# Kernel tuning notes

Measured on AMD Instinct MI355X. Metric: run time of the kernel, lower is better.

The kernel has to match this reference:

```python
import jax, jax.numpy as jnp
import numpy as np

MAX_GRAD = 200.0


@jax.custom_vjp
def sqrt_bound_derivative(x):
    return jnp.sqrt(x)


def _sqrt_bd_fwd(x):
    return jnp.sqrt(x), x


def _sqrt_bd_bwd(x, g):
    # derivative of sqrt clipped to MAX_GRAD: 0.5/sqrt(x) <= MAX_GRAD  <=>  x >= 1/(4*MAX_GRAD^2)
    x_clipped = jnp.maximum(x, 1.0 / (4.0 * MAX_GRAD * MAX_GRAD))
    return (g * 0.5 / jnp.sqrt(x_clipped),)


sqrt_bound_derivative.defvjp(_sqrt_bd_fwd, _sqrt_bd_bwd)


def linear_scan(a, x, h0):
    # h_t = a_t * h_{t-1} + x_t, diagonal recurrence over axis=1 (time).
    # Parallel form via associative scan on pairs (a, b): combine -> (a1*a2, a2*b1 + b2).
    def combine(c1, c2):
        a1, b1 = c1
        a2, b2 = c2
        return a1 * a2, a2 * b1 + b2

    a_cum, h = jax.lax.associative_scan(combine, (a, x), axis=1)
    # fold in initial state: h_t += (prod_{u<=t} a_u) * h0
    h = h + a_cum * h0[:, None, :]
    return h, h[:, -1]


def setup_inputs() -> dict:
    key = jax.random.key(0)
    ks = jax.random.split(key, 8)
    B, S, D_IN, D_HID, D_OUT = 8, 4096, 512, 1024, 512
    R_MIN, R_MAX = 0.9, 0.999

    x = jax.random.normal(ks[0], (B, S, D_IN), dtype=jnp.float32)
    h0 = jnp.zeros((B, D_HID), dtype=jnp.float32)

    # stable_init: a_logit = logit(U(r_min, r_max)) so that a = sigmoid(a_logit) in [r_min, r_max]
    u = jax.random.uniform(ks[1], (D_HID,), minval=R_MIN, maxval=R_MAX)
    a_logit = jnp.log(u) - jnp.log1p(-u)

    def dense_init(k, d_in, d_out):
        scale = 1.0 / np.sqrt(d_in)
        return jax.random.uniform(k, (d_in, d_out), minval=-scale, maxval=scale).astype(jnp.float32)

    W_dx = dense_init(ks[2], D_IN, D_OUT)
    b_dx = jnp.zeros((D_OUT,), dtype=jnp.float32)
    W_in = dense_init(ks[3], D_IN, D_HID)
    b_in = jnp.zeros((D_HID,), dtype=jnp.float32)
    W_out = dense_init(ks[4], D_HID, D_OUT)
    b_out = jnp.zeros((D_OUT,), dtype=jnp.float32)

    return {"x": x, "h0": h0, "a_logit": a_logit,
            "W_dx": W_dx, "b_dx": b_dx,
            "W_in": W_in, "b_in": b_in,
            "W_out": W_out, "b_out": b_out}


def reference(x, h0, a_logit, W_dx, b_dx, W_in, b_in, W_out, b_out):
    a = jax.nn.sigmoid(a_logit)                      # (d_hidden,)
    dx = jnp.einsum('bsi,io->bso', x, W_dx) + b_dx   # skip projection (b, s, d_out)
    u = jnp.einsum('bsi,ih->bsh', x, W_in) + b_in    # input projection (b, s, d_hidden)
    u = sqrt_bound_derivative(1.0 - a * a) * u       # input_norm gating
    a_b = jnp.broadcast_to(a, u.shape)
    h, h_last = linear_scan(a_b, u, h0)              # diagonal linear recurrence
    out = (dx + jnp.einsum('bsh,ho->bso', h, W_out) + b_out) / 2.0
    return out, h_last
```

## Files before the change

kernel.cpp:

```cpp
#include <hip/hip_runtime.h>

#define B_    8
#define S_    4096
#define DIN   512
#define DHID  1024
#define DOUT  512
#define M_    (B_*S_)
#define NCAT  (DHID + DOUT)
#define CH2   32
#define NCH2  (S_/CH2)

typedef __bf16 bf16x8 __attribute__((ext_vector_type(8)));
typedef float  floatx4 __attribute__((ext_vector_type(4)));

__device__ __forceinline__ unsigned short f2bf(float f) {
  unsigned u = __builtin_bit_cast(unsigned, f);
  u = (u + 0x7FFFu + ((u >> 16) & 1u)) >> 16;
  return (unsigned short)u;
}
__device__ __forceinline__ float bf2f(unsigned short h) {
  unsigned u = ((unsigned)h) << 16;
  return __builtin_bit_cast(float, u);
}

__device__ __forceinline__ void gl_lds16(const unsigned short* g, unsigned short* l) {
  __builtin_amdgcn_global_load_lds((const __attribute__((address_space(1))) void*)g,
                                   (__attribute__((address_space(3))) void*)l, 16, 0, 0);
}

__global__ void prep_all(const float* __restrict__ logit,
                         const float* __restrict__ Win, const float* __restrict__ Wdx,
                         const float* __restrict__ Wout, const float* __restrict__ x,
                         float* __restrict__ a_s,
                         unsigned short* __restrict__ wcat,
                         unsigned short* __restrict__ woutt,
                         unsigned short* __restrict__ xb) {
  int bx = blockIdx.x;
  if (bx < 3072) {
    int idx = bx * 256 + threadIdx.x;
    int n = idx >> 9, k = idx & 511;
    float v = (n < DHID) ? Win[(size_t)k * DHID + n] : Wdx[(size_t)k * DOUT + (n - DHID)];
    wcat[idx] = f2bf(v);
  } else if (bx < 5120) {
    int idx = (bx - 3072) * 256 + threadIdx.x;
    int n = idx >> 10, k = idx & 1023;
    woutt[idx] = f2bf(Wout[(size_t)k * DOUT + n]);
  } else if (bx < 5124) {
    int d = (bx - 5120) * 256 + threadIdx.x;
    if (d < DHID) {
      float a = 1.f / (1.f + expf(-logit[d]));
      a_s[d] = a;
      a_s[DHID + d] = sqrtf(fmaxf(1.f - a * a, 0.f));
    }
  } else {
    size_t i = (size_t)(bx - 5124) * 256 + threadIdx.x;
    const float4* p = (const float4*)x;
    float4 v0 = p[i * 2];
    float4 v1 = p[i * 2 + 1];
    uint4 o;
    o.x = (unsigned)f2bf(v0.x) | ((unsigned)f2bf(v0.y) << 16);
    o.y = (unsigned)f2bf(v0.z) | ((unsigned)f2bf(v0.w) << 16);
    o.z = (unsigned)f2bf(v1.x) | ((unsigned)f2bf(v1.y) << 16);
    o.w = (unsigned)f2bf(v1.z) | ((unsigned)f2bf(v1.w) << 16);
    *(uint4*)&xb[i * 8] = o;
  }
}

template <int K, int MODE, int NB>
__global__ __launch_bounds__(256, 4) void gemm_bt(
    const unsigned short* __restrict__ A,
    const unsigned short* __restrict__ Bt,
    const float* __restrict__ a_s,
    const float* __restrict__ bias0,
    const float* __restrict__ bias1,
    unsigned short* __restrict__ u_out,
    unsigned short* __restrict__ dx_buf,
    float* __restrict__ out,
    float* __restrict__ carry)
{
  __shared__ __align__(16) unsigned char smem[32768];
  unsigned short* lA = (unsigned short*)smem;
  unsigned short* lB = (unsigned short*)(smem + 16384);
  float* stg  = (float*)smem;
  float* ltmp = (float*)(smem + 16896);

  const int tid = threadIdx.x;
  const int flat = blockIdx.y * gridDim.x + blockIdx.x;
  const int xcd = flat & 7;
  const int j = flat >> 3;
  const int n0 = (j % NB) * 128;
  const int m0 = ((j / NB) * 8 + xcd) * 128;

  const int wid = tid >> 6, lane = tid & 63;
  const int wm = (wid >> 1) * 64, wn = (wid & 1) * 64;
  const int r16 = lane & 15, quad = lane >> 4;
  const int sw = r16 & 7;

  const int rsub = lane >> 3;
  const int gcol = ((lane & 7) ^ rsub) << 3;

  const unsigned short* Abase = A + (size_t)(m0 + (wid << 5) + rsub) * K + gcol;
  const unsigned short* Bbase = Bt + (size_t)(n0 + (wid << 5) + rsub) * K + gcol;
  unsigned short* lAw = lA + (wid << 5) * 64;
  unsigned short* lBw = lB + (wid << 5) * 64;

  floatx4 acc[4][4] = {};

  for (int k0 = 0; k0 < K; k0 += 64) {
#pragma unroll
    for (int i = 0; i < 4; ++i) {
      gl_lds16(Abase + (size_t)(i * 8) * K + k0, lAw + i * 8 * 64);
      gl_lds16(Bbase + (size_t)(i * 8) * K + k0, lBw + i * 8 * 64);
    }
    __syncthreads();
#pragma unroll
    for (int ks = 0; ks < 2; ++ks) {
      bf16x8 af[4], bfr[4];
#pragma unroll
      for (int i = 0; i < 4; ++i)
        af[i] = *(const bf16x8*)&lA[(wm + i * 16 + r16) * 64 + ((((ks << 2) | quad) ^ sw) << 3)];
#pragma unroll
      for (int j2 = 0; j2 < 4; ++j2)
        bfr[j2] = *(const bf16x8*)&lB[(wn + j2 * 16 + r16) * 64 + ((((ks << 2) | quad) ^ sw) << 3)];
#pragma unroll
      for (int i = 0; i < 4; ++i)
#pragma unroll
        for (int j2 = 0; j2 < 4; ++j2)
          acc[i][j2] = __builtin_amdgcn_mfma_f32_16x16x32_bf16(af[i], bfr[j2], acc[i][j2], 0, 0, 0);
    }
    __syncthreads();
  }

  const int row = tid >> 3;
  const int seg = tid & 7;
  const int scol_ = tid & 127;
  const int shalf = tid >> 7;
  float aa = 0.f, sbi = 0.f, ssc = 0.f, a16 = 0.f;
  if (MODE == 0 && n0 < DHID) {
    aa  = a_s[n0 + scol_];
    sbi = bias0[n0 + scol_];
    ssc = a_s[DHID + n0 + scol_];
    float t2 = aa * aa, t4 = t2 * t2, t8 = t4 * t4;
    a16 = t8 * t8;
  }
  const int bb = m0 >> 12;
  const int c0 = (m0 & 4095) >> 5;

#pragma unroll
  for (int p = 0; p < 4; ++p) {
    __syncthreads();
    if ((wid >> 1) == (p >> 1)) {
      const int i0 = (p & 1) * 2;
#pragma unroll
      for (int ii = 0; ii < 2; ++ii) {
        const int i = i0 + ii;
        const int srow = i * 16 + quad * 4 - (p & 1) * 32;
#pragma unroll
        for (int j2 = 0; j2 < 4; ++j2) {
          const int scol = wn + j2 * 16 + r16;
#pragma unroll
          for (int r = 0; r < 4; ++r)
            stg[(srow + r) * 132 + scol] = acc[i][j2][r];
        }
      }
    }
    __syncthreads();

    if (MODE == 0 && n0 < DHID) {
      float P = 0.f;
      const float* sp = &stg[(shalf * 16) * 132 + scol_];
#pragma unroll
      for (int r = 0; r < 16; ++r) {
        P = fmaf(aa, P, (sp[0] + sbi) * ssc);
        sp += 132;
      }
      if (shalf) ltmp[scol_] = P;
      __syncthreads();
      if (!shalf)
        carry[((size_t)bb * NCH2 + c0 + p) * DHID + n0 + scol_] = fmaf(a16, P, ltmp[scol_]);
    }

    const int gm = m0 + p * 32 + row;
    const int col0 = n0 + seg * 16;
    if (MODE == 0) {
      union { unsigned short s[16]; uint4 q[2]; } ub;
      if (n0 < DHID) {
#pragma unroll
        for (int u = 0; u < 4; ++u) {
          float4 v  = *(const float4*)&stg[row * 132 + seg * 16 + u * 4];
          float4 bi = *(const float4*)&bias0[col0 + u * 4];
          float4 sc = *(const float4*)&a_s[DHID + col0 + u * 4];
          ub.s[u * 4 + 0] = f2bf((v.x + bi.x) * sc.x);
          ub.s[u * 4 + 1] = f2bf((v.y + bi.y) * sc.y);
          ub.s[u * 4 + 2] = f2bf((v.z + bi.z) * sc.z);
          ub.s[u * 4 + 3] = f2bf((v.w + bi.w) * sc.w);
        }
        *(uint4*)&u_out[(size_t)gm * DHID + col0]     = ub.q[0];
        *(uint4*)&u_out[(size_t)gm * DHID + col0 + 8] = ub.q[1];
      } else {
        const int c2 = col0 - DHID;
#pragma unroll
        for (int u = 0; u < 4; ++u) {
          float4 v  = *(const float4*)&stg[row * 132 + seg * 16 + u * 4];
          float4 bd = *(const float4*)&bias1[c2 + u * 4];
          ub.s[u * 4 + 0] = f2bf(v.x + bd.x);
          ub.s[u * 4 + 1] = f2bf(v.y + bd.y);
          ub.s[u * 4 + 2] = f2bf(v.z + bd.z);
          ub.s[u * 4 + 3] = f2bf(v.w + bd.w);
        }
        *(uint4*)&dx_buf[(size_t)gm * DOUT + c2]     = ub.q[0];
        *(uint4*)&dx_buf[(size_t)gm * DOUT + c2 + 8] = ub.q[1];
      }
    } else {
#pragma unroll
      for (int u = 0; u < 4; ++u) {
        float4 v  = *(const float4*)&stg[row * 132 + seg * 16 + u * 4];
        float4 bo = *(const float4*)&bias0[col0 + u * 4];
        ushort4 dv = *(const ushort4*)&dx_buf[(size_t)gm * DOUT + col0 + u * 4];
        float4 o;
        o.x = (v.x + bo.x + bf2f(dv.x)) * 0.5f;
        o.y = (v.y + bo.y + bf2f(dv.y)) * 0.5f;
        o.z = (v.z + bo.z + bf2f(dv.z)) * 0.5f;
        o.w = (v.w + bo.w + bf2f(dv.w)) * 0.5f;
        *(float4*)&out[(size_t)gm * DOUT + col0 + u * 4] = o;
      }
    }
  }
}

__global__ __launch_bounds__(256) void scan_mid(const float* __restrict__ a_s,
                                                const float* __restrict__ h0,
                                                float* __restrict__ carry,
                                                float* __restrict__ h_last) {
  int idx = blockIdx.x * 256 + threadIdx.x;
  int d = idx & (DHID - 1);
  int b = idx >> 10;
  float a = a_s[d];
  float aL = a;
#pragma unroll
  for (int q = 0; q < 5; ++q) aL *= aL;
  float st = h0[(size_t)b * DHID + d];
  float* p = &carry[(size_t)b * NCH2 * DHID + d];
  for (int cg = 0; cg < NCH2; cg += 8) {
    float loc[8];
#pragma unroll
    for (int j = 0; j < 8; ++j) loc[j] = p[(size_t)j * DHID];
#pragma unroll
    for (int j = 0; j < 8; ++j) {
      p[(size_t)j * DHID] = st;
      st = fmaf(aL, st, loc[j]);
    }
    p += (size_t)8 * DHID;
  }
  h_last[(size_t)b * DHID + d] = st;
}

__global__ __launch_bounds__(256) void scan2(unsigned short* __restrict__ u,
                                             const float* __restrict__ a_s,
                                             const float* __restrict__ carry) {
  int idx = blockIdx.x * 256 + threadIdx.x;
  int d8 = (idx & 127) * 8;
  int c  = (idx >> 7) & (NCH2 - 1);
  int b  = idx >> 14;
  float4 a0 = *(const float4*)&a_s[d8];
  float4 a1 = *(const float4*)&a_s[d8 + 4];
  const float* cp = &carry[((size_t)(b * NCH2 + c)) * DHID + d8];
  float4 e0 = *(const float4*)cp;
  float4 e1 = *(const float4*)(cp + 4);
  float h0_ = e0.x, h1 = e0.y, h2 = e0.z, h3 = e0.w;
  float h4 = e1.x, h5 = e1.y, h6 = e1.z, h7 = e1.w;
  unsigned short* up = u + ((size_t)(b * S_ + c * CH2)) * DHID + d8;
#pragma unroll 4
  for (int t = 0; t < CH2; ++t) {
    ushort4 q0 = *(const ushort4*)up;
    ushort4 q1 = *(const ushort4*)(up + 4);
    h0_ = fmaf(a0.x, h0_, bf2f(q0.x)); h1 = fmaf(a0.y, h1, bf2f(q0.y));
    h2  = fmaf(a0.z, h2,  bf2f(q0.z)); h3 = fmaf(a0.w, h3, bf2f(q0.w));
    h4  = fmaf(a1.x, h4,  bf2f(q1.x)); h5 = fmaf(a1.y, h5, bf2f(q1.y));
    h6  = fmaf(a1.z, h6,  bf2f(q1.z)); h7 = fmaf(a1.w, h7, bf2f(q1.w));
    ushort4 w0, w1;
    w0.x = f2bf(h0_); w0.y = f2bf(h1); w0.z = f2bf(h2); w0.w = f2bf(h3);
    w1.x = f2bf(h4);  w1.y = f2bf(h5); w1.z = f2bf(h6); w1.w = f2bf(h7);
    *(ushort4*)up = w0;
    *(ushort4*)(up + 4) = w1;
    up += DHID;
  }
}

extern "C" void kernel_launch(void* const* d_in, const int* in_sizes, int n_in,
                              void* d_out, int out_size, void* d_ws, size_t ws_size,
                              hipStream_t stream) {
  const float* x    = (const float*)d_in[0];
  const float* h0   = (const float*)d_in[1];
  const float* alog = (const float*)d_in[2];
  const float* Wdx  = (const float*)d_in[3];
  const float* bdx  = (const float*)d_in[4];
  const float* Win  = (const float*)d_in[5];
  const float* bin  = (const float*)d_in[6];
  const float* Wout = (const float*)d_in[7];
  const float* bout = (const float*)d_in[8];

  float* out    = (float*)d_out;
  float* h_last = out + (size_t)M_ * DOUT;

  char* ws = (char*)d_ws;
  unsigned short* xb    = (unsigned short*)(ws);
  unsigned short* ubuf  = (unsigned short*)(ws + 33554432ull);
  unsigned short* dxb   = (unsigned short*)(ws + 100663296ull);
  unsigned short* wcat  = (unsigned short*)(ws + 134217728ull);
  unsigned short* woutt = (unsigned short*)(ws + 135790592ull);
  float*          a_s   = (float*)(ws + 136839168ull);
  float*          carry = (float*)(ws + 136847360ull);

  prep_all<<<5124 + (M_ * DIN / 8) / 256, 256, 0, stream>>>(
      alog, Win, Wdx, Wout, x, a_s, wcat, woutt, xb);

  gemm_bt<DIN, 0, 12><<<dim3(NCAT / 128, M_ / 128), 256, 0, stream>>>(
      xb, wcat, a_s, bin, bdx, ubuf, dxb, nullptr, carry);

  scan_mid<<<(B_ * DHID) / 256, 256, 0, stream>>>(a_s, h0, carry, h_last);
  scan2   <<<(B_ * NCH2 * (DHID / 8)) / 256, 256, 0, stream>>>(ubuf, a_s, carry);

  gemm_bt<DHID, 1, 4><<<dim3(DOUT / 128, M_ / 128), 256, 0, stream>>>(
      ubuf, woutt, a_s, bout, nullptr, nullptr, dxb, out, nullptr);
}
```

Baseline: 283.3 us.

## Replace first GEMM with 256x256-tile, 512-thread, 4-stage pipelined kernel

Adds a dedicated first-projection kernel that uses 256x256 output tiles with 8 waves, a 4-slot direct global-to-LDS staging pipeline and swizzled LDS reads. Its block index is remapped so that neighbouring blocks share tiles for better cache locality. The epilogue stages results through LDS in four passes to compute the chunk carries and write bf16 u/dx. The goal is more data reuse per loaded byte and better overlap of memory with MFMA work, at the cost of 128KB LDS per block and heavy register use, which lower occupancy.

Result: no change. 278.5 us (-1.7%).

```diff
diff --git a/kernel.cpp b/kernel.cpp
--- a/kernel.cpp
+++ b/kernel.cpp
@@ -63,6 +63,178 @@
     o.z = (unsigned)f2bf(v1.x) | ((unsigned)f2bf(v1.y) << 16);
     o.w = (unsigned)f2bf(v1.z) | ((unsigned)f2bf(v1.w) << 16);
     *(uint4*)&xb[i * 8] = o;
+  }
+}
+
+__global__ __launch_bounds__(512, 2) void gemm1(
+    const unsigned short* __restrict__ A,
+    const unsigned short* __restrict__ Bt,
+    const float* __restrict__ a_s,
+    const float* __restrict__ bin,
+    const float* __restrict__ bdx,
+    unsigned short* __restrict__ u_out,
+    unsigned short* __restrict__ dx_buf,
+    float* __restrict__ carry)
+{
+  __shared__ __align__(16) unsigned char smem[131072];
+
+  const int tid  = threadIdx.x;
+  const int lane = tid & 63, wid = tid >> 6;
+  const int r16  = lane & 15, quad = lane >> 4;
+  const int wm = (wid >> 2) * 128, wn = (wid & 3) * 64;
+  const int csw = (quad ^ ((r16 >> 1) & 3)) << 4;
+
+  const int flat = blockIdx.x;
+  const int jj = (flat & 7) * 96 + (flat >> 3);
+  const int nt = jj % 6, mt = jj / 6;
+  const int n0 = nt * 256, m0 = mt * 256;
+
+  const unsigned oA0 = (unsigned)wid * 1024u + (unsigned)lane * 16u;
+  const unsigned oA1 = oA0 + 8192u;
+  const int rA0 = oA0 >> 6, cA0 = (int)((oA0 >> 4) & 3u) ^ ((rA0 >> 1) & 3);
+  const int rA1 = oA1 >> 6, cA1 = (int)((oA1 >> 4) & 3u) ^ ((rA1 >> 1) & 3);
+  const unsigned short* sA0 = A  + (size_t)(m0 + rA0) * DIN + cA0 * 8;
+  const unsigned short* sA1 = A  + (size_t)(m0 + rA1) * DIN + cA1 * 8;
+  const unsigned short* sB0 = Bt + (size_t)(n0 + rA0) * DIN + cA0 * 8;
+  const unsigned short* sB1 = Bt + (size_t)(n0 + rA1) * DIN + cA1 * 8;
+
+  unsigned char* lds = smem;
+  const unsigned dA0 = (unsigned)wid * 1024u, dA1 = dA0 + 8192u;
+
+  floatx4 acc[8][4] = {};
+
+  auto stage = [&](int slot, int kt) {
+    unsigned char* d = lds + slot * 32768;
+    const int ko = kt * 32;
+    gl_lds16(sA0 + ko, (unsigned short*)(d + dA0));
+    gl_lds16(sA1 + ko, (unsigned short*)(d + dA1));
+    gl_lds16(sB0 + ko, (unsigned short*)(d + 16384 + dA0));
+    gl_lds16(sB1 + ko, (unsigned short*)(d + 16384 + dA1));
+  };
+
+  auto compute = [&](int slot) {
+    const unsigned char* pA = lds + slot * 32768;
+    const unsigned char* pB = pA + 16384;
+    bf16x8 af[8], bfr[4];
+#pragma unroll
+    for (int j = 0; j < 4; ++j)
+      bfr[j] = *(const bf16x8*)(pB + (wn + j * 16 + r16) * 64 + csw);
+#pragma unroll
+    for (int i = 0; i < 8; ++i)
+      af[i] = *(const bf16x8*)(pA + (wm + i * 16 + r16) * 64 + csw);
+    __builtin_amdgcn_s_setprio(1);
+#pragma unroll
+    for (int i = 0; i < 8; ++i)
+#pragma unroll
+      for (int j = 0; j < 4; ++j)
+        acc[i][j] = __builtin_amdgcn_mfma_f32_16x16x32_bf16(af[i], bfr[j], acc[i][j], 0, 0, 0);
+    __builtin_amdgcn_s_setprio(0);
+  };
+
+  stage(0, 0); stage(1, 1); stage(2, 2);
+  asm volatile("s_waitcnt vmcnt(8)" ::: "memory");
+  __builtin_amdgcn_s_barrier();
+
+  for (int t = 0; t < 13; ++t) {
+    stage((t + 3) & 3, t + 3);
+    compute(t & 3);
+    asm volatile("s_waitcnt vmcnt(8) lgkmcnt(0)" ::: "memory");
+    __builtin_amdgcn_s_barrier();
+  }
+  compute(1);
+  asm volatile("s_waitcnt vmcnt(4) lgkmcnt(0)" ::: "memory");
+  __builtin_amdgcn_s_barrier();
+  compute(2);
+  asm volatile("s_waitcnt vmcnt(0) lgkmcnt(0)" ::: "memory");
+  __builtin_amdgcn_s_barrier();
+  compute(3);
+  asm volatile("s_waitcnt lgkmcnt(0)" ::: "memory");
+  __builtin_amdgcn_s_barrier();
+
+  float* stg = (float*)smem;
+  const bool isU = (n0 < DHID);
+
+  const int sg = tid & 31, rw0 = tid >> 5;
+  const int colS = tid & 255, ch = tid >> 8;
+
+  float aa = 0.f, sbi = 0.f, ssc = 0.f;
+  float4 bv0, bv1, sv0, sv1;
+  if (isU) {
+    aa  = a_s[n0 + colS];
+    sbi = bin[n0 + colS];
+    ssc = a_s[DHID + n0 + colS];
+    bv0 = *(const float4*)&bin[n0 + sg * 8];
+    bv1 = *(const float4*)&bin[n0 + sg * 8 + 4];
+    sv0 = *(const float4*)&a_s[DHID + n0 + sg * 8];
+    sv1 = *(const float4*)&a_s[DHID + n0 + sg * 8 + 4];
+  } else {
+    bv0 = *(const float4*)&bdx[n0 - DHID + sg * 8];
+    bv1 = *(const float4*)&bdx[n0 - DHID + sg * 8 + 4];
+    sv0 = bv0; sv1 = bv1;
+  }
+
+#pragma unroll
+  for (int p = 0; p < 4; ++p) {
+    if ((wid >> 2) == (p >> 1)) {
+      const int ib = (p & 1) * 4;
+#pragma unroll
+      for (int ii = 0; ii < 4; ++ii) {
+#pragma unroll
+        for (int j = 0; j < 4; ++j) {
+          const int col = (wid & 3) * 64 + j * 16 + r16;
+#pragma unroll
+          for (int r = 0; r < 4; ++r)
+            stg[(ii * 16 + quad * 4 + r) * 260 + col] = acc[ib + ii][j][r];
+        }
+      }
+    }
+    asm volatile("s_waitcnt lgkmcnt(0)" ::: "memory");
+    __builtin_amdgcn_s_barrier();
+
+    const int gmb = m0 + p * 64;
+    if (isU) {
+      float P = 0.f;
+      const float* sp = &stg[(ch * 32) * 260 + colS];
+#pragma unroll
+      for (int r = 0; r < 32; ++r) { P = fmaf(aa, P, (sp[0] + sbi) * ssc); sp += 260; }
+      const int gm0 = gmb + ch * 32;
+      carry[((size_t)(gm0 >> 12) * NCH2 + ((gm0 & 4095) >> 5)) * DHID + n0 + colS] = P;
+#pragma unroll
+      for (int q = 0; q < 4; ++q) {
+        const int lr = rw0 + q * 16;
+        float4 v0 = *(const float4*)&stg[lr * 260 + sg * 8];
+        float4 v1 = *(const float4*)&stg[lr * 260 + sg * 8 + 4];
+        union { unsigned short s[8]; uint4 u4; } ub;
+        ub.s[0] = f2bf((v0.x + bv0.x) * sv0.x);
+        ub.s[1] = f2bf((v0.y + bv0.y) * sv0.y);
+        ub.s[2] = f2bf((v0.z + bv0.z) * sv0.z);
+        ub.s[3] = f2bf((v0.w + bv0.w) * sv0.w);
+        ub.s[4] = f2bf((v1.x + bv1.x) * sv1.x);
+        ub.s[5] = f2bf((v1.y + bv1.y) * sv1.y);
+        ub.s[6] = f2bf((v1.z + bv1.z) * sv1.z);
+        ub.s[7] = f2bf((v1.w + bv1.w) * sv1.w);
+        *(uint4*)&u_out[(size_t)(gmb + lr) * DHID + n0 + sg * 8] = ub.u4;
+      }
+    } else {
+#pragma unroll
+      for (int q = 0; q < 4; ++q) {
+        const int lr = rw0 + q * 16;
+        float4 v0 = *(const float4*)&stg[lr * 260 + sg * 8];
+        float4 v1 = *(const float4*)&stg[lr * 260 + sg * 8 + 4];
+        union { unsigned short s[8]; uint4 u4; } ub;
+        ub.s[0] = f2bf(v0.x + bv0.x);
+        ub.s[1] = f2bf(v0.y + bv0.y);
+        ub.s[2] = f2bf(v0.z + bv0.z);
+        ub.s[3] = f2bf(v0.w + bv0.w);
+        ub.s[4] = f2bf(v1.x + bv1.x);
+        ub.s[5] = f2bf(v1.y + bv1.y);
+        ub.s[6] = f2bf(v1.z + bv1.z);
+        ub.s[7] = f2bf(v1.w + bv1.w);
+        *(uint4*)&dx_buf[(size_t)(gmb + lr) * DOUT + (n0 - DHID) + sg * 8] = ub.u4;
+      }
+    }
+    asm volatile("s_waitcnt lgkmcnt(0)" ::: "memory");
+    __builtin_amdgcn_s_barrier();
   }
 }
 
@@ -315,8 +487,8 @@
   prep_all<<<5124 + (M_ * DIN / 8) / 256, 256, 0, stream>>>(
       alog, Win, Wdx, Wout, x, a_s, wcat, woutt, xb);
 
-  gemm_bt<DIN, 0, 12><<<dim3(NCAT / 128, M_ / 128), 256, 0, stream>>>(
-      xb, wcat, a_s, bin, bdx, ubuf, dxb, nullptr, carry);
+  gemm1<<<dim3((M_ / 256) * (NCAT / 256)), dim3(512), 0, stream>>>(
+      xb, wcat, a_s, bin, bdx, ubuf, dxb, carry);
 
   scan_mid<<<(B_ * DHID) / 256, 256, 0, stream>>>(a_s, h0, carry, h_last);
   scan2   <<<(B_ * NCH2 * (DHID / 8)) / 256, 256, 0, stream>>>(ubuf, a_s, carry);
```

## Replace 128x128 GEMM with 256x256 tile, 4-stage LDS pipelined kernel

Applied to the files above, without the earlier changes.

Both GEMMs move from a 128x128 tile with 256 threads to a 256x256 tile with 512 threads (8 waves). K-slices of 32 are loaded into a 4-deep LDS ring, staged three slices ahead, with hand-placed barriers, vmcnt waits and setprio around the MFMA bursts. The epilogue is rewritten for the larger tile, and the per-chunk carry is now computed by one thread over 32 rows. The aim is more data reuse per tile and better overlap of global loads with MFMA, at the cost of 128KB LDS per block, lower occupancy, and fragile manual synchronisation.

Measured after the change: 270.2 us. -4.6%, faster.

```diff
diff --git a/kernel.cpp b/kernel.cpp
--- a/kernel.cpp
+++ b/kernel.cpp
@@ -66,8 +66,8 @@
   }
 }
 
-template <int K, int MODE, int NB>
-__global__ __launch_bounds__(256, 4) void gemm_bt(
+template <int K, int MODE, int NTN>
+__global__ __launch_bounds__(512, 2) void gemm256(
     const unsigned short* __restrict__ A,
     const unsigned short* __restrict__ Bt,
     const float* __restrict__ a_s,
@@ -75,156 +75,185 @@
     const float* __restrict__ bias1,
     unsigned short* __restrict__ u_out,
     unsigned short* __restrict__ dx_buf,
+    const unsigned short* __restrict__ dx_in,
     float* __restrict__ out,
     float* __restrict__ carry)
 {
-  __shared__ __align__(16) unsigned char smem[32768];
-  unsigned short* lA = (unsigned short*)smem;
-  unsigned short* lB = (unsigned short*)(smem + 16384);
-  float* stg  = (float*)smem;
-  float* ltmp = (float*)(smem + 16896);
-
-  const int tid = threadIdx.x;
-  const int flat = blockIdx.y * gridDim.x + blockIdx.x;
-  const int xcd = flat & 7;
-  const int j = flat >> 3;
-  const int n0 = (j % NB) * 128;
-  const int m0 = ((j / NB) * 8 + xcd) * 128;
-
-  const int wid = tid >> 6, lane = tid & 63;
-  const int wm = (wid >> 1) * 64, wn = (wid & 1) * 64;
-  const int r16 = lane & 15, quad = lane >> 4;
-  const int sw = r16 & 7;
-
-  const int rsub = lane >> 3;
-  const int gcol = ((lane & 7) ^ rsub) << 3;
-
-  const unsigned short* Abase = A + (size_t)(m0 + (wid << 5) + rsub) * K + gcol;
-  const unsigned short* Bbase = Bt + (size_t)(n0 + (wid << 5) + rsub) * K + gcol;
-  unsigned short* lAw = lA + (wid << 5) * 64;
-  unsigned short* lBw = lB + (wid << 5) * 64;
-
-  floatx4 acc[4][4] = {};
-
-  for (int k0 = 0; k0 < K; k0 += 64) {
-#pragma unroll
-    for (int i = 0; i < 4; ++i) {
-      gl_lds16(Abase + (size_t)(i * 8) * K + k0, lAw + i * 8 * 64);
-      gl_lds16(Bbase + (size_t)(i * 8) * K + k0, lBw + i * 8 * 64);
+  constexpr int NG = K / 32;
+  __shared__ __align__(16) unsigned char smem[131072];
+  unsigned char* lds = smem;
+
+  const int tid  = threadIdx.x;
+  const int lane = tid & 63, wid = tid >> 6;
+  const int r16  = lane & 15, quad = lane >> 4;
+  const int wm = (wid >> 2) * 128, wn = (wid & 3) * 64;
+  const int csw = (quad ^ ((r16 >> 1) & 3)) << 4;
+
+  constexpr int TOT = (M_ / 256) * NTN;
+  const int flat = blockIdx.x;
+  const int jj = (flat & 7) * (TOT / 8) + (flat >> 3);
+  const int nt = jj % NTN, mt = jj / NTN;
+  const int n0 = nt * 256, m0 = mt * 256;
+
+  const int srow = (wid << 4) + (lane >> 2);
+  const int scol = ((lane & 3) ^ ((lane >> 3) & 3)) << 3;
+  const unsigned short* gA0 = A  + (size_t)(m0 + srow) * K + scol;
+  const unsigned short* gB0 = Bt + (size_t)(n0 + srow) * K + scol;
+  const unsigned oA = (unsigned)wid * 1024u + (unsigned)lane * 16u;
+
+  floatx4 acc[8][4] = {};
+  bf16x8 af[4], bf[4];
+
+  auto stageA = [&](int g) {
+    unsigned short* d = (unsigned short*)(lds + (g & 3) * 32768 + oA);
+    const unsigned short* s = gA0 + (size_t)g * 32;
+    gl_lds16(s, d);
+    gl_lds16(s + (size_t)128 * K, d + 4096);
+  };
+  auto stageB = [&](int g) {
+    unsigned short* d = (unsigned short*)(lds + (g & 3) * 32768 + 16384 + oA);
+    const unsigned short* s = gB0 + (size_t)g * 32;
+    gl_lds16(s, d);
+    gl_lds16(s + (size_t)128 * K, d + 4096);
+  };
+
+  auto phA = [&](int g, int gs, bool st) {
+    const unsigned char* sl = lds + (g & 3) * 32768;
+#pragma unroll
+    for (int j = 0; j < 4; ++j)
+      bf[j] = *(const bf16x8*)(sl + 16384 + (wn + j * 16 + r16) * 64 + csw);
+#pragma unroll
+    for (int i = 0; i < 4; ++i)
+      af[i] = *(const bf16x8*)(sl + (wm + i * 16 + r16) * 64 + csw);
+    if (st) stageA(gs);
+    asm volatile("s_barrier" ::: "memory");
+    asm volatile("s_waitcnt lgkmcnt(0)" ::: "memory");
+    __builtin_amdgcn_sched_barrier(0);
+    __builtin_amdgcn_s_setprio(1);
+#pragma unroll
+    for (int i = 0; i < 4; ++i)
+#pragma unroll
+      for (int j = 0; j < 4; ++j)
+        acc[i][j] = __builtin_amdgcn_mfma_f32_16x16x32_bf16(af[i], bf[j], acc[i][j], 0, 0, 0);
+    __builtin_amdgcn_s_setprio(0);
+    asm volatile("s_barrier" ::: "memory");
+  };
+  auto phB = [&](int g, int gs, bool st) {
+    const unsigned char* sl = lds + (g & 3) * 32768;
+#pragma unroll
+    for (int i = 0; i < 4; ++i)
+      af[i] = *(const bf16x8*)(sl + (wm + (4 + i) * 16 + r16) * 64 + csw);
+    if (st) stageB(gs);
+    asm volatile("s_barrier" ::: "memory");
+    asm volatile("s_waitcnt lgkmcnt(0)" ::: "memory");
+    __builtin_amdgcn_sched_barrier(0);
+    __builtin_amdgcn_s_setprio(1);
+#pragma unroll
+    for (int i = 0; i < 4; ++i)
+#pragma unroll
+      for (int j = 0; j < 4; ++j)
+        acc[4 + i][j] = __builtin_amdgcn_mfma_f32_16x16x32_bf16(af[i], bf[j], acc[4 + i][j], 0, 0, 0);
+    __builtin_amdgcn_s_setprio(0);
+  };
+
+  stageA(0); stageB(0); stageA(1); stageB(1); stageA(2); stageB(2);
+  asm volatile("s_waitcnt vmcnt(8)" ::: "memory");
+  asm volatile("s_barrier" ::: "memory");
+
+  for (int g = 0; g < NG - 3; ++g) {
+    phA(g, g + 3, true);
+    phB(g, g + 3, true);
+    asm volatile("s_waitcnt vmcnt(8)" ::: "memory");
+    asm volatile("s_barrier" ::: "memory");
+  }
+  phA(NG - 3, 0, false); phB(NG - 3, 0, false);
+  asm volatile("s_waitcnt vmcnt(4)" ::: "memory");
+  asm volatile("s_barrier" ::: "memory");
+  phA(NG - 2, 0, false); phB(NG - 2, 0, false);
+  asm volatile("s_waitcnt vmcnt(0)" ::: "memory");
+  asm volatile("s_barrier" ::: "memory");
+  phA(NG - 1, 0, false); phB(NG - 1, 0, false);
+  asm volatile("s_barrier" ::: "memory");
+
+  float* stg = (float*)smem;
+  const bool isU = (MODE == 0) && (n0 < DHID);
+  const int c4 = lane << 2;
+
+  float4 bv = {}, sv = {};
+  if (MODE == 0) {
+    if (isU) { bv = *(const float4*)&bias0[n0 + c4]; sv = *(const float4*)&a_s[DHID + n0 + c4]; }
+    else     { bv = *(const float4*)&bias1[(n0 - DHID) + c4]; }
+  } else {
+    bv = *(const float4*)&bias0[n0 + c4];
+  }
+
+  const int colS = tid & 255, ch = tid >> 8;
+  float aa = 0.f, sbi = 0.f, ssc = 0.f;
+  if (isU) { aa = a_s[n0 + colS]; sbi = bias0[n0 + colS]; ssc = a_s[DHID + n0 + colS]; }
+
+#pragma unroll
+  for (int p = 0; p < 4; ++p) {
+    if ((wid >> 2) == (p >> 1)) {
+      const int ib = (p & 1) * 4;
+#pragma unroll
+      for (int ii = 0; ii < 4; ++ii)
+#pragma unroll
+        for (int j = 0; j < 4; ++j) {
+          const int col = (wid & 3) * 64 + j * 16 + r16;
+#pragma unroll
+          for (int r = 0; r < 4; ++r)
+            stg[(ii * 16 + quad * 4 + r) * 260 + col] = acc[ib + ii][j][r];
+        }
     }
-    __syncthreads();
-#pragma unroll
-    for (int ks = 0; ks < 2; ++ks) {
-      bf16x8 af[4], bfr[4];
-#pragma unroll
-      for (int i = 0; i < 4; ++i)
-        af[i] = *(const bf16x8*)&lA[(wm + i * 16 + r16) * 64 + ((((ks << 2) | quad) ^ sw) << 3)];
-#pragma unroll
-      for (int j2 = 0; j2 < 4; ++j2)
-        bfr[j2] = *(const bf16x8*)&lB[(wn + j2 * 16 + r16) * 64 + ((((ks << 2) | quad) ^ sw) << 3)];
-#pragma unroll
-      for (int i = 0; i < 4; ++i)
-#pragma unroll
-        for (int j2 = 0; j2 < 4; ++j2)
-          acc[i][j2] = __builtin_amdgcn_mfma_f32_16x16x32_bf16(af[i], bfr[j2], acc[i][j2], 0, 0, 0);
-    }
-    __syncthreads();
-  }
-
-  const int row = tid >> 3;
-  const int seg = tid & 7;
-  const int scol_ = tid & 127;
-  const int shalf = tid >> 7;
-  float aa = 0.f, sbi = 0.f, ssc = 0.f, a16 = 0.f;
-  if (MODE == 0 && n0 < DHID) {
-    aa  = a_s[n0 + scol_];
-    sbi = bias0[n0 + scol_];
-    ssc = a_s[DHID + n0 + scol_];
-    float t2 = aa * aa, t4 = t2 * t2, t8 = t4 * t4;
-    a16 = t8 * t8;
-  }
-  const int bb = m0 >> 12;
-  const int c0 = (m0 & 4095) >> 5;
-
-#pragma unroll
-  for (int p = 0; p < 4; ++p) {
-    __syncthreads();
-    if ((wid >> 1) == (p >> 1)) {
-      const int i0 = (p & 1) * 2;
-#pragma unroll
-      for (int ii = 0; ii < 2; ++ii) {
-        const int i = i0 + ii;
-        const int srow = i * 16 + quad * 4 - (p & 1) * 32;
-#pragma unroll
-        for (int j2 = 0; j2 < 4; ++j2) {
-          const int scol = wn + j2 * 16 + r16;
-#pragma unroll
-          for (int r = 0; r < 4; ++r)
-            stg[(srow + r) * 132 + scol] = acc[i][j2][r];
-        }
+    asm volatile("s_waitcnt lgkmcnt(0)" ::: "memory");
+    asm volatile("s_barrier" ::: "memory");
+
+    const int gmb = m0 + p * 64;
+    if (isU) {
+      float P = 0.f;
+      const float* sp = &stg[(ch * 32) * 260 + colS];
+#pragma unroll
+      for (int r = 0; r < 32; ++r) { P = fmaf(aa, P, (sp[0] + sbi) * ssc); sp += 260; }
+      const int gm0 = gmb + ch * 32;
+      carry[((size_t)(gm0 >> 12) * NCH2 + ((gm0 & 4095) >> 5)) * DHID + n0 + colS] = P;
+#pragma unroll
+      for (int rr = 0; rr < 8; ++rr) {
+        const int lr = (wid << 3) + rr;
+        float4 v = *(const float4*)&stg[lr * 260 + c4];
+        ushort4 o;
+        o.x = f2bf((v.x + bv.x) * sv.x);
+        o.y = f2bf((v.y + bv.y) * sv.y);
+        o.z = f2bf((v.z + bv.z) * sv.z);
+        o.w = f2bf((v.w + bv.w) * sv.w);
+        *(ushort4*)&u_out[(size_t)(gmb + lr) * DHID + n0 + c4] = o;
+      }
+    } else if (MODE == 0) {
+#pragma unroll
+      for (int rr = 0; rr < 8; ++rr) {
+        const int lr = (wid << 3) + rr;
+        float4 v = *(const float4*)&stg[lr * 260 + c4];
+        ushort4 o;
+        o.x = f2bf(v.x + bv.x);
+        o.y = f2bf(v.y + bv.y);
+        o.z = f2bf(v.z + bv.z);
+        o.w = f2bf(v.w + bv.w);
+        *(ushort4*)&dx_buf[(size_t)(gmb + lr) * DOUT + (n0 - DHID) + c4] = o;
+      }
+    } else {
+#pragma unroll
+      for (int rr = 0; rr < 8; ++rr) {
+        const int lr = (wid << 3) + rr;
+        float4 v = *(const float4*)&stg[lr * 260 + c4];
+        ushort4 dv = *(const ushort4*)&dx_in[(size_t)(gmb + lr) * DOUT + n0 + c4];
+        float4 o;
+        o.x = (v.x + bv.x + bf2f(dv.x)) * 0.5f;
+        o.y = (v.y + bv.y + bf2f(dv.y)) * 0.5f;
+        o.z = (v.z + bv.z + bf2f(dv.z)) * 0.5f;
+        o.w = (v.w + bv.w + bf2f(dv.w)) * 0.5f;
+        *(float4*)&out[(size_t)(gmb + lr) * DOUT + n0 + c4] = o;
       }
     }
-    __syncthreads();
-
-    if (MODE == 0 && n0 < DHID) {
-      float P = 0.f;
-      const float* sp = &stg[(shalf * 16) * 132 + scol_];
-#pragma unroll
-      for (int r = 0; r < 16; ++r) {
-        P = fmaf(aa, P, (sp[0] + sbi) * ssc);
-        sp += 132;
-      }
-      if (shalf) ltmp[scol_] = P;
-      __syncthreads();
-      if (!shalf)
-        carry[((size_t)bb * NCH2 + c0 + p) * DHID + n0 + scol_] = fmaf(a16, P, ltmp[scol_]);
-    }
-
-    const int gm = m0 + p * 32 + row;
-    const int col0 = n0 + seg * 16;
-    if (MODE == 0) {
-      union { unsigned short s[16]; uint4 q[2]; } ub;
-      if (n0 < DHID) {
-#pragma unroll
-        for (int u = 0; u < 4; ++u) {
-          float4 v  = *(const float4*)&stg[row * 132 + seg * 16 + u * 4];
-          float4 bi = *(const float4*)&bias0[col0 + u * 4];
-          float4 sc = *(const float4*)&a_s[DHID + col0 + u * 4];
-          ub.s[u * 4 + 0] = f2bf((v.x + bi.x) * sc.x);
-          ub.s[u * 4 + 1] = f2bf((v.y + bi.y) * sc.y);
-          ub.s[u * 4 + 2] = f2bf((v.z + bi.z) * sc.z);
-          ub.s[u * 4 + 3] = f2bf((v.w + bi.w) * sc.w);
-        }
-        *(uint4*)&u_out[(size_t)gm * DHID + col0]     = ub.q[0];
-        *(uint4*)&u_out[(size_t)gm * DHID + col0 + 8] = ub.q[1];
-      } else {
-        const int c2 = col0 - DHID;
-#pragma unroll
-        for (int u = 0; u < 4; ++u) {
-          float4 v  = *(const float4*)&stg[row * 132 + seg * 16 + u * 4];
-          float4 bd = *(const float4*)&bias1[c2 + u * 4];
-          ub.s[u * 4 + 0] = f2bf(v.x + bd.x);
-          ub.s[u * 4 + 1] = f2bf(v.y + bd.y);
-          ub.s[u * 4 + 2] = f2bf(v.z + bd.z);
-          ub.s[u * 4 + 3] = f2bf(v.w + bd.w);
-        }
-        *(uint4*)&dx_buf[(size_t)gm * DOUT + c2]     = ub.q[0];
-        *(uint4*)&dx_buf[(size_t)gm * DOUT + c2 + 8] = ub.q[1];
-      }
-    } else {
-#pragma unroll
-      for (int u = 0; u < 4; ++u) {
-        float4 v  = *(const float4*)&stg[row * 132 + seg * 16 + u * 4];
-        float4 bo = *(const float4*)&bias0[col0 + u * 4];
-        ushort4 dv = *(const ushort4*)&dx_buf[(size_t)gm * DOUT + col0 + u * 4];
-        float4 o;
-        o.x = (v.x + bo.x + bf2f(dv.x)) * 0.5f;
-        o.y = (v.y + bo.y + bf2f(dv.y)) * 0.5f;
-        o.z = (v.z + bo.z + bf2f(dv.z)) * 0.5f;
-        o.w = (v.w + bo.w + bf2f(dv.w)) * 0.5f;
-        *(float4*)&out[(size_t)gm * DOUT + col0 + u * 4] = o;
-      }
-    }
+    asm volatile("s_barrier" ::: "memory");
   }
 }
 
@@ -315,12 +344,12 @@
   prep_all<<<5124 + (M_ * DIN / 8) / 256, 256, 0, stream>>>(
       alog, Win, Wdx, Wout, x, a_s, wcat, woutt, xb);
 
-  gemm_bt<DIN, 0, 12><<<dim3(NCAT / 128, M_ / 128), 256, 0, stream>>>(
-      xb, wcat, a_s, bin, bdx, ubuf, dxb, nullptr, carry);
+  gemm256<DIN, 0, 6><<<dim3((M_ / 256) * 6), dim3(512), 0, stream>>>(
+      xb, wcat, a_s, bin, bdx, ubuf, dxb, nullptr, nullptr, carry);
 
   scan_mid<<<(B_ * DHID) / 256, 256, 0, stream>>>(a_s, h0, carry, h_last);
   scan2   <<<(B_ * NCH2 * (DHID / 8)) / 256, 256, 0, stream>>>(ubuf, a_s, carry);
 
-  gemm_bt<DHID, 1, 4><<<dim3(DOUT / 128, M_ / 128), 256, 0, stream>>>(
-      ubuf, woutt, a_s, bout, nullptr, nullptr, dxb, out, nullptr);
-}
+  gemm256<DHID, 1, 2><<<dim3((M_ / 256) * 2), dim3(512), 0, stream>>>(
+      ubuf, woutt, a_s, bout, nullptr, nullptr, nullptr, dxb, out, nullptr);
+}
```
